# Kernel optimization log

Measured on AMD Instinct MI355X. Metric: run time of the kernel, lower is better.

Reference implementation:

```python
import jax, jax.numpy as jnp
import numpy as np

NA = 100000   # node_num_a
NB = 100000   # node_num_b
D = 128       # a_dim == b_dim
E = 1_600_000 # edges, avg degree 16


def setup_inputs() -> dict:
    key = jax.random.key(0)
    k1, k2, k3, k4, k5, k6 = jax.random.split(key, 6)
    feature_a = jax.random.normal(k1, (NA, D), dtype=jnp.float32)
    feature_b = jax.random.normal(k2, (NB, D), dtype=jnp.float32)
    src = jax.random.randint(k3, (E, 1), 0, NA)
    dst = jax.random.randint(k4, (E, 1), 0, NB)
    edges = jnp.concatenate([src, dst], axis=1).astype(jnp.int64)
    W_mlp = jax.random.normal(k5, (D, D), dtype=jnp.float32) / np.sqrt(D)
    b_mlp = jnp.zeros((D,), dtype=jnp.float32)
    a_vec = jax.random.normal(k6, (2 * D, 1), dtype=jnp.float32) / np.sqrt(2 * D)
    return {"feature_a": feature_a, "feature_b": feature_b, "edges": edges,
            "W_mlp": W_mlp, "b_mlp": b_mlp, "a_vec": a_vec}


def reference(feature_a, feature_b, edges, W_mlp, b_mlp, a_vec):
    """AttentionAggregator.forward: edge-gathered attention + segment aggregation."""
    na, a_dim = feature_a.shape
    # nn.Linear: x @ W.T + b
    new_emb = feature_b @ W_mlp.T + b_mlp                      # [Nb, D]
    # einsum(cat([fa[src], new_emb[dst]]), a) == fa[src]@a_top + new_emb[dst]@a_bot
    a_top = a_vec[:a_dim, 0]
    a_bot = a_vec[a_dim:, 0]
    s_a = feature_a @ a_top                                    # [Na]
    s_b = new_emb @ a_bot                                      # [Nb]
    src = edges[:, 0]
    dst = edges[:, 1]
    score = s_a[src] + s_b[dst]                                # [E]
    # F.elu(x, alpha=0.1) then exp
    ALPHA = 0.1
    elu = jnp.where(score > 0, score, ALPHA * jnp.expm1(score))
    w = jnp.exp(elu)                                           # [E]
    # sparse.mm(matrix, ones)  -> per-row sum of edge weights (duplicates coalesce by sum)
    row_sum = jax.ops.segment_sum(w, src, num_segments=na)     # [Na]
    row_sum = jnp.where(row_sum == 0, 1.0, row_sum)
    # sparse.mm(matrix, new_emb) -> weighted neighbor aggregation
    msg = w[:, None] * new_emb[dst]                            # [E, D]
    agg = jax.ops.segment_sum(msg, src, num_segments=na)       # [Na, D]
    return agg / row_sum[:, None]
```

## Files before the change

### kernel.cpp

```cpp
#include <hip/hip_runtime.h>
#include <math.h>

#define NA 100000
#define NB 100000
#define DIM 128
#define NEDGE 1600000
#define ALPHA 0.1f

#define WS_NEBF   0
#define WS_WBF    25600000
#define WS_SA     25632768
#define WS_SB     26032768
#define WS_DEG    26432768
#define WS_FLAG   26832768
#define WS_OFF    26832832
#define WS_CUR    27232832
#define WS_PAIRS  27632832

using bf16x8 = __attribute__((ext_vector_type(8))) short;
using f32x16 = __attribute__((ext_vector_type(16))) float;

__device__ inline short f2bf(float f) {
    union { float f; unsigned u; } v; v.f = f;
    const unsigned r = (v.u + 0x7FFFu + ((v.u >> 16) & 1u)) >> 16;
    return (short)r;
}

__global__ void k_prep(const int* __restrict__ edges32, int* __restrict__ flags,
                       const float* __restrict__ W, short* __restrict__ wbf) {
    if (blockIdx.x == 0) {
        __shared__ int any;
        if (threadIdx.x == 0) any = 0;
        __syncthreads();
        if (edges32[2 * threadIdx.x + 1] != 0) atomicOr(&any, 1);
        __syncthreads();
        if (threadIdx.x == 0) flags[0] = (any == 0) ? 1 : 0;
    } else {
        const int i = (blockIdx.x - 1) * 256 + threadIdx.x;
        if (i < DIM * DIM) wbf[i] = f2bf(W[i]);
    }
}

__global__ __launch_bounds__(256) void k_newemb(
    const float* __restrict__ fb, const short* __restrict__ wbf,
    const float* __restrict__ bias, const float* __restrict__ avec,
    short* __restrict__ nebf, float* __restrict__ s_b)
{
    const int wv = threadIdx.x >> 6;
    const int lane = threadIdx.x & 63;
    const int tile = blockIdx.x * 4 + wv;
    const int row0 = tile * 32;
    if (row0 >= NB) return;
    const int l31 = lane & 31;
    const int h = lane >> 5;

    f32x16 acc[4];
    #pragma unroll
    for (int nt = 0; nt < 4; ++nt)
        #pragma unroll
        for (int r = 0; r < 16; ++r) acc[nt][r] = 0.f;

    const float* arow = fb + (size_t)(row0 + l31) * DIM;

    #pragma unroll 2
    for (int s = 0; s < 8; ++s) {
        const int k0 = s * 16 + h * 8;
        const float4 a0 = *(const float4*)(arow + k0);
        const float4 a1 = *(const float4*)(arow + k0 + 4);
        bf16x8 af;
        af[0] = f2bf(a0.x); af[1] = f2bf(a0.y); af[2] = f2bf(a0.z); af[3] = f2bf(a0.w);
        af[4] = f2bf(a1.x); af[5] = f2bf(a1.y); af[6] = f2bf(a1.z); af[7] = f2bf(a1.w);
        #pragma unroll
        for (int nt = 0; nt < 4; ++nt) {
            const int n = nt * 32 + l31;
            const bf16x8 bf = *(const bf16x8*)(wbf + n * DIM + k0);
            acc[nt] = __builtin_amdgcn_mfma_f32_32x32x16_bf16(af, bf, acc[nt], 0, 0, 0);
        }
    }

    float ab[4], bs[4];
    #pragma unroll
    for (int nt = 0; nt < 4; ++nt) {
        ab[nt] = avec[DIM + nt * 32 + l31];
        bs[nt] = bias[nt * 32 + l31];
    }
    float sb[16];
    #pragma unroll
    for (int r = 0; r < 16; ++r) {
        const int row = row0 + (r & 3) + 8 * (r >> 2) + 4 * h;
        float p = 0.f;
        #pragma unroll
        for (int nt = 0; nt < 4; ++nt) {
            const float v = acc[nt][r] + bs[nt];
            nebf[(size_t)row * DIM + nt * 32 + l31] = f2bf(v);
            p += v * ab[nt];
        }
        #pragma unroll
        for (int m = 16; m; m >>= 1) p += __shfl_xor(p, m, 64);
        sb[r] = p;
    }
    if (l31 == 0) {
        #pragma unroll
        for (int r = 0; r < 16; ++r)
            s_b[row0 + (r & 3) + 8 * (r >> 2) + 4 * h] = sb[r];
    }
}

__global__ __launch_bounds__(256) void k_sa(
    const float* __restrict__ fa, const float* __restrict__ avec,
    float* __restrict__ s_a)
{
    const int row = blockIdx.x * 4 + (threadIdx.x >> 6);
    if (row >= NA) return;
    const int lane = threadIdx.x & 63;
    const float2 v = *(const float2*)(fa + (size_t)row * DIM + 2 * lane);
    const float2 a = *(const float2*)(avec + 2 * lane);
    float p = v.x * a.x + v.y * a.y;
    #pragma unroll
    for (int m = 32; m; m >>= 1) p += __shfl_xor(p, m, 64);
    if (lane == 0) s_a[row] = p;
}

__global__ __launch_bounds__(256) void k_hist(
    const void* __restrict__ edges, const int* __restrict__ flags,
    int* __restrict__ deg)
{
    const int e = blockIdx.x * 256 + threadIdx.x;
    if (e >= NEDGE) return;
    int src;
    if (flags[0]) src = (int)((const long long*)edges)[2 * (size_t)e];
    else          src = ((const int2*)edges)[e].x;
    atomicAdd(&deg[src], 1);
}

__global__ __launch_bounds__(256) void k_off(
    const int* __restrict__ deg, int* __restrict__ offs, int* __restrict__ cur,
    int* __restrict__ flags)
{
    const int lane = threadIdx.x & 63;
    const int w = blockIdx.x * 4 + (threadIdx.x >> 6);
    const int r = w * 64 + lane;
    const int d = (r < NA) ? deg[r] : 0;
    int incl = d;
    #pragma unroll
    for (int m = 1; m < 64; m <<= 1) {
        const int t = __shfl_up(incl, m, 64);
        if (lane >= m) incl += t;
    }
    int base = 0;
    if (lane == 63) base = atomicAdd(&flags[1], incl);
    base = __shfl(base, 63, 64);
    if (r < NA) {
        const int o = base + incl - d;
        offs[r] = o;
        cur[r] = o;
    }
}

__global__ __launch_bounds__(256) void k_place(
    const void* __restrict__ edges, const int* __restrict__ flags,
    const float* __restrict__ s_a, const float* __restrict__ s_b,
    int* __restrict__ cur, int2* __restrict__ pairs)
{
    const int e = blockIdx.x * 256 + threadIdx.x;
    if (e >= NEDGE) return;
    int src, dst;
    if (flags[0]) {
        const long long* p = (const long long*)edges;
        src = (int)p[2 * (size_t)e];
        dst = (int)p[2 * (size_t)e + 1];
    } else {
        const int2 ed = ((const int2*)edges)[e];
        src = ed.x; dst = ed.y;
    }
    const float sc = s_a[src] + s_b[dst];
    const float el = (sc > 0.f) ? sc : ALPHA * expm1f(sc);
    const float w = expf(el);
    const int pos = atomicAdd(&cur[src], 1);
    if ((unsigned)pos < NEDGE)
        pairs[pos] = make_int2(dst, __float_as_int(w));
}

#define ACC8(u, wt)                                                             \
    a0 += (wt) * __uint_as_float((u).x << 16);                                  \
    a1 += (wt) * __uint_as_float((u).x & 0xFFFF0000u);                          \
    a2 += (wt) * __uint_as_float((u).y << 16);                                  \
    a3 += (wt) * __uint_as_float((u).y & 0xFFFF0000u);                          \
    a4 += (wt) * __uint_as_float((u).z << 16);                                  \
    a5 += (wt) * __uint_as_float((u).z & 0xFFFF0000u);                          \
    a6 += (wt) * __uint_as_float((u).w << 16);                                  \
    a7 += (wt) * __uint_as_float((u).w & 0xFFFF0000u);

__global__ __launch_bounds__(256) void k_rowagg(
    const int* __restrict__ deg, const int* __restrict__ offs,
    const int2* __restrict__ pairs, const unsigned* __restrict__ nebf,
    float* __restrict__ out)
{
    const int row = blockIdx.x * 4 + (threadIdx.x >> 6);
    if (row >= NA) return;
    const int lane = threadIdx.x & 63;
    const int l = lane & 15;
    const int q = lane >> 4;
    const int cnt = deg[row];
    const int2* bucket = pairs + offs[row];

    float a0 = 0.f, a1 = 0.f, a2 = 0.f, a3 = 0.f;
    float a4 = 0.f, a5 = 0.f, a6 = 0.f, a7 = 0.f, wsum = 0.f;
    int i = q;
    for (; i + 4 < cnt; i += 8) {
        const int2 p0 = bucket[i];
        const int2 p1 = bucket[i + 4];
        const uint4 u0 = *(const uint4*)(nebf + (size_t)p0.x * (DIM / 2) + 4 * l);
        const uint4 u1 = *(const uint4*)(nebf + (size_t)p1.x * (DIM / 2) + 4 * l);
        const float w0 = __int_as_float(p0.y);
        const float w1 = __int_as_float(p1.y);
        ACC8(u0, w0)
        ACC8(u1, w1)
        wsum += w0 + w1;
    }
    for (; i < cnt; i += 4) {
        const int2 p = bucket[i];
        const uint4 u = *(const uint4*)(nebf + (size_t)p.x * (DIM / 2) + 4 * l);
        const float wv = __int_as_float(p.y);
        ACC8(u, wv)
        wsum += wv;
    }
    a0 += __shfl_xor(a0, 16, 64); a0 += __shfl_xor(a0, 32, 64);
    a1 += __shfl_xor(a1, 16, 64); a1 += __shfl_xor(a1, 32, 64);
    a2 += __shfl_xor(a2, 16, 64); a2 += __shfl_xor(a2, 32, 64);
    a3 += __shfl_xor(a3, 16, 64); a3 += __shfl_xor(a3, 32, 64);
    a4 += __shfl_xor(a4, 16, 64); a4 += __shfl_xor(a4, 32, 64);
    a5 += __shfl_xor(a5, 16, 64); a5 += __shfl_xor(a5, 32, 64);
    a6 += __shfl_xor(a6, 16, 64); a6 += __shfl_xor(a6, 32, 64);
    a7 += __shfl_xor(a7, 16, 64); a7 += __shfl_xor(a7, 32, 64);
    wsum += __shfl_xor(wsum, 16, 64); wsum += __shfl_xor(wsum, 32, 64);
    if (q == 0) {
        const float inv = 1.f / ((wsum == 0.f) ? 1.f : wsum);
        float* o = out + (size_t)row * DIM + 8 * l;
        *(float4*)o       = make_float4(a0 * inv, a1 * inv, a2 * inv, a3 * inv);
        *(float4*)(o + 4) = make_float4(a4 * inv, a5 * inv, a6 * inv, a7 * inv);
    }
}

extern "C" void kernel_launch(void* const* d_in, const int* in_sizes, int n_in,
                              void* d_out, int out_size, void* d_ws, size_t ws_size,
                              hipStream_t stream) {
    const float* fa    = (const float*)d_in[0];
    const float* fb    = (const float*)d_in[1];
    const void*  edges = d_in[2];
    const float* W     = (const float*)d_in[3];
    const float* bias  = (const float*)d_in[4];
    const float* avec  = (const float*)d_in[5];
    float* out = (float*)d_out;
    char* ws = (char*)d_ws;
    short* nebf = (short*)(ws + WS_NEBF);
    short* wbf  = (short*)(ws + WS_WBF);
    float* s_a  = (float*)(ws + WS_SA);
    float* s_b  = (float*)(ws + WS_SB);
    int*   deg  = (int*)(ws + WS_DEG);
    int*   flags= (int*)(ws + WS_FLAG);
    int*   offs = (int*)(ws + WS_OFF);
    int*   cur  = (int*)(ws + WS_CUR);
    int2*  pairs= (int2*)(ws + WS_PAIRS);

    (void)hipMemsetAsync(ws + WS_DEG, 0, (size_t)NA * sizeof(int) + 64, stream);
    k_prep<<<1 + (DIM * DIM + 255) / 256, 256, 0, stream>>>((const int*)edges, flags, W, wbf);
    k_newemb<<<(NB / 32 + 3) / 4, 256, 0, stream>>>(fb, wbf, bias, avec, nebf, s_b);
    k_sa<<<(NA + 3) / 4, 256, 0, stream>>>(fa, avec, s_a);
    k_hist<<<(NEDGE + 255) / 256, 256, 0, stream>>>(edges, flags, deg);
    k_off<<<(NA + 255) / 256, 256, 0, stream>>>(deg, offs, cur, flags);
    k_place<<<(NEDGE + 255) / 256, 256, 0, stream>>>(edges, flags, s_a, s_b, cur, pairs);
    k_rowagg<<<(NA + 3) / 4, 256, 0, stream>>>(deg, offs, pairs, (const unsigned*)nebf, out);
}
```

Baseline: 410.6 us.

## Fuse newemb, s_a and histogram kernels; drop cursor array; batch edges per thread

Result: slower. 446.6 us (+8.8%).

```diff
diff --git a/kernel.cpp b/kernel.cpp
--- a/kernel.cpp
+++ b/kernel.cpp
@@ -14,8 +14,14 @@
 #define WS_DEG    26432768
 #define WS_FLAG   26832768
 #define WS_OFF    26832832
-#define WS_CUR    27232832
-#define WS_PAIRS  27632832
+#define WS_PAIRS  27232832
+
+#define NEWEMB_BLOCKS 782
+#define SA_BLOCKS     25000
+#define EPT_H 8
+#define HIST_BLOCKS   782
+#define EPT_P 4
+#define PLACE_BLOCKS  1563
 
 using bf16x8 = __attribute__((ext_vector_type(8))) short;
 using f32x16 = __attribute__((ext_vector_type(16))) float;
@@ -41,101 +47,106 @@
     }
 }
 
-__global__ __launch_bounds__(256) void k_newemb(
+__global__ __launch_bounds__(256) void k_fused(
     const float* __restrict__ fb, const short* __restrict__ wbf,
     const float* __restrict__ bias, const float* __restrict__ avec,
-    short* __restrict__ nebf, float* __restrict__ s_b)
-{
-    const int wv = threadIdx.x >> 6;
-    const int lane = threadIdx.x & 63;
-    const int tile = blockIdx.x * 4 + wv;
-    const int row0 = tile * 32;
-    if (row0 >= NB) return;
-    const int l31 = lane & 31;
-    const int h = lane >> 5;
-
-    f32x16 acc[4];
-    #pragma unroll
-    for (int nt = 0; nt < 4; ++nt)
-        #pragma unroll
-        for (int r = 0; r < 16; ++r) acc[nt][r] = 0.f;
-
-    const float* arow = fb + (size_t)(row0 + l31) * DIM;
-
-    #pragma unroll 2
-    for (int s = 0; s < 8; ++s) {
-        const int k0 = s * 16 + h * 8;
-        const float4 a0 = *(const float4*)(arow + k0);
-        const float4 a1 = *(const float4*)(arow + k0 + 4);
-        bf16x8 af;
-        af[0] = f2bf(a0.x); af[1] = f2bf(a0.y); af[2] = f2bf(a0.z); af[3] = f2bf(a0.w);
-        af[4] = f2bf(a1.x); af[5] = f2bf(a1.y); af[6] = f2bf(a1.z); af[7] = f2bf(a1.w);
-        #pragma unroll
-        for (int nt = 0; nt < 4; ++nt) {
-            const int n = nt * 32 + l31;
-            const bf16x8 bf = *(const bf16x8*)(wbf + n * DIM + k0);
-            acc[nt] = __builtin_amdgcn_mfma_f32_32x32x16_bf16(af, bf, acc[nt], 0, 0, 0);
-        }
-    }
-
-    float ab[4], bs[4];
-    #pragma unroll
-    for (int nt = 0; nt < 4; ++nt) {
-        ab[nt] = avec[DIM + nt * 32 + l31];
-        bs[nt] = bias[nt * 32 + l31];
-    }
-    float sb[16];
-    #pragma unroll
-    for (int r = 0; r < 16; ++r) {
-        const int row = row0 + (r & 3) + 8 * (r >> 2) + 4 * h;
-        float p = 0.f;
-        #pragma unroll
-        for (int nt = 0; nt < 4; ++nt) {
-            const float v = acc[nt][r] + bs[nt];
-            nebf[(size_t)row * DIM + nt * 32 + l31] = f2bf(v);
-            p += v * ab[nt];
-        }
-        #pragma unroll
-        for (int m = 16; m; m >>= 1) p += __shfl_xor(p, m, 64);
-        sb[r] = p;
-    }
-    if (l31 == 0) {
-        #pragma unroll
-        for (int r = 0; r < 16; ++r)
-            s_b[row0 + (r & 3) + 8 * (r >> 2) + 4 * h] = sb[r];
-    }
-}
-
-__global__ __launch_bounds__(256) void k_sa(
-    const float* __restrict__ fa, const float* __restrict__ avec,
-    float* __restrict__ s_a)
-{
-    const int row = blockIdx.x * 4 + (threadIdx.x >> 6);
-    if (row >= NA) return;
-    const int lane = threadIdx.x & 63;
-    const float2 v = *(const float2*)(fa + (size_t)row * DIM + 2 * lane);
-    const float2 a = *(const float2*)(avec + 2 * lane);
-    float p = v.x * a.x + v.y * a.y;
-    #pragma unroll
-    for (int m = 32; m; m >>= 1) p += __shfl_xor(p, m, 64);
-    if (lane == 0) s_a[row] = p;
-}
-
-__global__ __launch_bounds__(256) void k_hist(
+    short* __restrict__ nebf, float* __restrict__ s_b,
+    const float* __restrict__ fa, float* __restrict__ s_a,
     const void* __restrict__ edges, const int* __restrict__ flags,
     int* __restrict__ deg)
 {
-    const int e = blockIdx.x * 256 + threadIdx.x;
-    if (e >= NEDGE) return;
-    int src;
-    if (flags[0]) src = (int)((const long long*)edges)[2 * (size_t)e];
-    else          src = ((const int2*)edges)[e].x;
-    atomicAdd(&deg[src], 1);
+    const int lane = threadIdx.x & 63;
+    if (blockIdx.x < NEWEMB_BLOCKS) {
+        const int wv = threadIdx.x >> 6;
+        const int tile = blockIdx.x * 4 + wv;
+        const int row0 = tile * 32;
+        if (row0 >= NB) return;
+        const int l31 = lane & 31;
+        const int h = lane >> 5;
+
+        f32x16 acc[4];
+        #pragma unroll
+        for (int nt = 0; nt < 4; ++nt)
+            #pragma unroll
+            for (int r = 0; r < 16; ++r) acc[nt][r] = 0.f;
+
+        const float* arow = fb + (size_t)(row0 + l31) * DIM;
+
+        #pragma unroll 2
+        for (int s = 0; s < 8; ++s) {
+            const int k0 = s * 16 + h * 8;
+            const float4 a0 = *(const float4*)(arow + k0);
+            const float4 a1 = *(const float4*)(arow + k0 + 4);
+            bf16x8 af;
+            af[0] = f2bf(a0.x); af[1] = f2bf(a0.y); af[2] = f2bf(a0.z); af[3] = f2bf(a0.w);
+            af[4] = f2bf(a1.x); af[5] = f2bf(a1.y); af[6] = f2bf(a1.z); af[7] = f2bf(a1.w);
+            #pragma unroll
+            for (int nt = 0; nt < 4; ++nt) {
+                const int n = nt * 32 + l31;
+                const bf16x8 bf = *(const bf16x8*)(wbf + n * DIM + k0);
+                acc[nt] = __builtin_amdgcn_mfma_f32_32x32x16_bf16(af, bf, acc[nt], 0, 0, 0);
+            }
+        }
+
+        float ab[4], bs[4];
+        #pragma unroll
+        for (int nt = 0; nt < 4; ++nt) {
+            ab[nt] = avec[DIM + nt * 32 + l31];
+            bs[nt] = bias[nt * 32 + l31];
+        }
+        float sb[16];
+        #pragma unroll
+        for (int r = 0; r < 16; ++r) {
+            const int row = row0 + (r & 3) + 8 * (r >> 2) + 4 * h;
+            float p = 0.f;
+            #pragma unroll
+            for (int nt = 0; nt < 4; ++nt) {
+                const float v = acc[nt][r] + bs[nt];
+                nebf[(size_t)row * DIM + nt * 32 + l31] = f2bf(v);
+                p += v * ab[nt];
+            }
+            #pragma unroll
+            for (int m = 16; m; m >>= 1) p += __shfl_xor(p, m, 64);
+            sb[r] = p;
+        }
+        if (l31 == 0) {
+            #pragma unroll
+            for (int r = 0; r < 16; ++r)
+                s_b[row0 + (r & 3) + 8 * (r >> 2) + 4 * h] = sb[r];
+        }
+    } else if (blockIdx.x < NEWEMB_BLOCKS + SA_BLOCKS) {
+        const int row = (blockIdx.x - NEWEMB_BLOCKS) * 4 + (threadIdx.x >> 6);
+        if (row >= NA) return;
+        const float2 v = *(const float2*)(fa + (size_t)row * DIM + 2 * lane);
+        const float2 a = *(const float2*)(avec + 2 * lane);
+        float p = v.x * a.x + v.y * a.y;
+        #pragma unroll
+        for (int m = 32; m; m >>= 1) p += __shfl_xor(p, m, 64);
+        if (lane == 0) s_a[row] = p;
+    } else {
+        const int t = (blockIdx.x - NEWEMB_BLOCKS - SA_BLOCKS) * 256 + threadIdx.x;
+        const long long e0 = (long long)t * EPT_H;
+        if (e0 >= NEDGE) return;
+        if (flags[0]) {
+            const int4* p = (const int4*)edges;
+            int s[EPT_H];
+            #pragma unroll
+            for (int k = 0; k < EPT_H; ++k) s[k] = p[e0 + k].x;
+            #pragma unroll
+            for (int k = 0; k < EPT_H; ++k) atomicAdd(&deg[s[k]], 1);
+        } else {
+            const int2* p = (const int2*)edges;
+            int s[EPT_H];
+            #pragma unroll
+            for (int k = 0; k < EPT_H; ++k) s[k] = p[e0 + k].x;
+            #pragma unroll
+            for (int k = 0; k < EPT_H; ++k) atomicAdd(&deg[s[k]], 1);
+        }
+    }
 }
 
 __global__ __launch_bounds__(256) void k_off(
-    const int* __restrict__ deg, int* __restrict__ offs, int* __restrict__ cur,
-    int* __restrict__ flags)
+    const int* __restrict__ deg, int* __restrict__ offs, int* __restrict__ flags)
 {
     const int lane = threadIdx.x & 63;
     const int w = blockIdx.x * 4 + (threadIdx.x >> 6);
@@ -150,35 +161,41 @@
     int base = 0;
     if (lane == 63) base = atomicAdd(&flags[1], incl);
     base = __shfl(base, 63, 64);
-    if (r < NA) {
-        const int o = base + incl - d;
-        offs[r] = o;
-        cur[r] = o;
-    }
+    if (r < NA) offs[r] = base + incl - d;
 }
 
 __global__ __launch_bounds__(256) void k_place(
     const void* __restrict__ edges, const int* __restrict__ flags,
     const float* __restrict__ s_a, const float* __restrict__ s_b,
-    int* __restrict__ cur, int2* __restrict__ pairs)
-{
-    const int e = blockIdx.x * 256 + threadIdx.x;
-    if (e >= NEDGE) return;
-    int src, dst;
+    int* __restrict__ offs, int2* __restrict__ pairs)
+{
+    const int t = blockIdx.x * 256 + threadIdx.x;
+    const long long e0 = (long long)t * EPT_P;
+    if (e0 >= NEDGE) return;
+    int src[EPT_P], dst[EPT_P];
     if (flags[0]) {
-        const long long* p = (const long long*)edges;
-        src = (int)p[2 * (size_t)e];
-        dst = (int)p[2 * (size_t)e + 1];
+        const int4* p = (const int4*)edges;
+        #pragma unroll
+        for (int k = 0; k < EPT_P; ++k) { const int4 v = p[e0 + k]; src[k] = v.x; dst[k] = v.z; }
     } else {
-        const int2 ed = ((const int2*)edges)[e];
-        src = ed.x; dst = ed.y;
-    }
-    const float sc = s_a[src] + s_b[dst];
-    const float el = (sc > 0.f) ? sc : ALPHA * expm1f(sc);
-    const float w = expf(el);
-    const int pos = atomicAdd(&cur[src], 1);
-    if ((unsigned)pos < NEDGE)
-        pairs[pos] = make_int2(dst, __float_as_int(w));
+        const int2* p = (const int2*)edges;
+        #pragma unroll
+        for (int k = 0; k < EPT_P; ++k) { const int2 v = p[e0 + k]; src[k] = v.x; dst[k] = v.y; }
+    }
+    float w[EPT_P];
+    #pragma unroll
+    for (int k = 0; k < EPT_P; ++k) {
+        const float sc = s_a[src[k]] + s_b[dst[k]];
+        const float el = (sc > 0.f) ? sc : ALPHA * expm1f(sc);
+        w[k] = expf(el);
+    }
+    int pos[EPT_P];
+    #pragma unroll
+    for (int k = 0; k < EPT_P; ++k) pos[k] = atomicAdd(&offs[src[k]], 1);
+    #pragma unroll
+    for (int k = 0; k < EPT_P; ++k)
+        if ((unsigned)pos[k] < NEDGE)
+            pairs[pos[k]] = make_int2(dst[k], __float_as_int(w[k]));
 }
 
 #define ACC8(u, wt)                                                             \
@@ -202,7 +219,7 @@
     const int l = lane & 15;
     const int q = lane >> 4;
     const int cnt = deg[row];
-    const int2* bucket = pairs + offs[row];
+    const int2* bucket = pairs + (offs[row] - cnt);
 
     float a0 = 0.f, a1 = 0.f, a2 = 0.f, a3 = 0.f;
     float a4 = 0.f, a5 = 0.f, a6 = 0.f, a7 = 0.f, wsum = 0.f;
@@ -260,15 +277,13 @@
     int*   deg  = (int*)(ws + WS_DEG);
     int*   flags= (int*)(ws + WS_FLAG);
     int*   offs = (int*)(ws + WS_OFF);
-    int*   cur  = (int*)(ws + WS_CUR);
     int2*  pairs= (int2*)(ws + WS_PAIRS);
 
     (void)hipMemsetAsync(ws + WS_DEG, 0, (size_t)NA * sizeof(int) + 64, stream);
     k_prep<<<1 + (DIM * DIM + 255) / 256, 256, 0, stream>>>((const int*)edges, flags, W, wbf);
-    k_newemb<<<(NB / 32 + 3) / 4, 256, 0, stream>>>(fb, wbf, bias, avec, nebf, s_b);
-    k_sa<<<(NA + 3) / 4, 256, 0, stream>>>(fa, avec, s_a);
-    k_hist<<<(NEDGE + 255) / 256, 256, 0, stream>>>(edges, flags, deg);
-    k_off<<<(NA + 255) / 256, 256, 0, stream>>>(deg, offs, cur, flags);
-    k_place<<<(NEDGE + 255) / 256, 256, 0, stream>>>(edges, flags, s_a, s_b, cur, pairs);
+    k_fused<<<NEWEMB_BLOCKS + SA_BLOCKS + HIST_BLOCKS, 256, 0, stream>>>(
+        fb, wbf, bias, avec, nebf, s_b, fa, s_a, edges, flags, deg);
+    k_off<<<(NA + 255) / 256, 256, 0, stream>>>(deg, offs, flags);
+    k_place<<<PLACE_BLOCKS, 256, 0, stream>>>(edges, flags, s_a, s_b, offs, pairs);
     k_rowagg<<<(NA + 3) / 4, 256, 0, stream>>>(deg, offs, pairs, (const unsigned*)nebf, out);
 }
```

## Replace CSR build with fixed-capacity per-row buckets and overflow list

Applied to the files above, without the earlier changes.

Result: slower. 424.8 us (+3.4%).

```diff
diff --git a/kernel.cpp b/kernel.cpp
--- a/kernel.cpp
+++ b/kernel.cpp
@@ -6,16 +6,20 @@
 #define DIM 128
 #define NEDGE 1600000
 #define ALPHA 0.1f
+#define BCAP 31
+#define OVF_CAP 65536
 
 #define WS_NEBF   0
 #define WS_WBF    25600000
 #define WS_SA     25632768
 #define WS_SB     26032768
-#define WS_DEG    26432768
+#define WS_CNT    26432768
 #define WS_FLAG   26832768
-#define WS_OFF    26832832
-#define WS_CUR    27232832
-#define WS_PAIRS  27632832
+#define WS_OVF    26832832
+#define WS_PAIRS  27357120
+
+#define EPT_P 4
+#define SCAT_BLOCKS 1563
 
 using bf16x8 = __attribute__((ext_vector_type(8))) short;
 using f32x16 = __attribute__((ext_vector_type(16))) float;
@@ -121,64 +125,36 @@
     if (lane == 0) s_a[row] = p;
 }
 
-__global__ __launch_bounds__(256) void k_hist(
+__global__ __launch_bounds__(256) void k_scatter(
     const void* __restrict__ edges, const int* __restrict__ flags,
-    int* __restrict__ deg)
-{
-    const int e = blockIdx.x * 256 + threadIdx.x;
-    if (e >= NEDGE) return;
-    int src;
-    if (flags[0]) src = (int)((const long long*)edges)[2 * (size_t)e];
-    else          src = ((const int2*)edges)[e].x;
-    atomicAdd(&deg[src], 1);
-}
-
-__global__ __launch_bounds__(256) void k_off(
-    const int* __restrict__ deg, int* __restrict__ offs, int* __restrict__ cur,
-    int* __restrict__ flags)
-{
-    const int lane = threadIdx.x & 63;
-    const int w = blockIdx.x * 4 + (threadIdx.x >> 6);
-    const int r = w * 64 + lane;
-    const int d = (r < NA) ? deg[r] : 0;
-    int incl = d;
-    #pragma unroll
-    for (int m = 1; m < 64; m <<= 1) {
-        const int t = __shfl_up(incl, m, 64);
-        if (lane >= m) incl += t;
-    }
-    int base = 0;
-    if (lane == 63) base = atomicAdd(&flags[1], incl);
-    base = __shfl(base, 63, 64);
-    if (r < NA) {
-        const int o = base + incl - d;
-        offs[r] = o;
-        cur[r] = o;
-    }
-}
-
-__global__ __launch_bounds__(256) void k_place(
-    const void* __restrict__ edges, const int* __restrict__ flags,
-    const float* __restrict__ s_a, const float* __restrict__ s_b,
-    int* __restrict__ cur, int2* __restrict__ pairs)
-{
-    const int e = blockIdx.x * 256 + threadIdx.x;
-    if (e >= NEDGE) return;
-    int src, dst;
+    int* __restrict__ cnt, int* __restrict__ bucket,
+    int2* __restrict__ ovf, int* __restrict__ ovfcnt)
+{
+    const int t = blockIdx.x * 256 + threadIdx.x;
+    const long long e0 = (long long)t * EPT_P;
+    if (e0 >= NEDGE) return;
+    int src[EPT_P], dst[EPT_P];
     if (flags[0]) {
-        const long long* p = (const long long*)edges;
-        src = (int)p[2 * (size_t)e];
-        dst = (int)p[2 * (size_t)e + 1];
+        const int4* p = (const int4*)edges;
+        #pragma unroll
+        for (int k = 0; k < EPT_P; ++k) { const int4 v = p[e0 + k]; src[k] = v.x; dst[k] = v.z; }
     } else {
-        const int2 ed = ((const int2*)edges)[e];
-        src = ed.x; dst = ed.y;
-    }
-    const float sc = s_a[src] + s_b[dst];
-    const float el = (sc > 0.f) ? sc : ALPHA * expm1f(sc);
-    const float w = expf(el);
-    const int pos = atomicAdd(&cur[src], 1);
-    if ((unsigned)pos < NEDGE)
-        pairs[pos] = make_int2(dst, __float_as_int(w));
+        const int2* p = (const int2*)edges;
+        #pragma unroll
+        for (int k = 0; k < EPT_P; ++k) { const int2 v = p[e0 + k]; src[k] = v.x; dst[k] = v.y; }
+    }
+    int pos[EPT_P];
+    #pragma unroll
+    for (int k = 0; k < EPT_P; ++k) pos[k] = atomicAdd(&cnt[src[k]], 1);
+    #pragma unroll
+    for (int k = 0; k < EPT_P; ++k) {
+        if (pos[k] < BCAP) {
+            bucket[src[k] * BCAP + pos[k]] = dst[k];
+        } else {
+            const int o = atomicAdd(ovfcnt, 1);
+            if (o < OVF_CAP) ovf[o] = make_int2(src[k], dst[k]);
+        }
+    }
 }
 
 #define ACC8(u, wt)                                                             \
@@ -191,39 +167,59 @@
     a6 += (wt) * __uint_as_float((u).w << 16);                                  \
     a7 += (wt) * __uint_as_float((u).w & 0xFFFF0000u);
 
+__device__ inline float edge_w(float sar, float sb) {
+    const float sc = sar + sb;
+    const float el = (sc > 0.f) ? sc : ALPHA * expm1f(sc);
+    return expf(el);
+}
+
 __global__ __launch_bounds__(256) void k_rowagg(
-    const int* __restrict__ deg, const int* __restrict__ offs,
-    const int2* __restrict__ pairs, const unsigned* __restrict__ nebf,
-    float* __restrict__ out)
+    const int* __restrict__ cnt, const int* __restrict__ bucket_all,
+    const float* __restrict__ s_a, const float* __restrict__ s_b,
+    const unsigned* __restrict__ nebf, const int2* __restrict__ ovf,
+    const int* __restrict__ flags, float* __restrict__ out)
 {
     const int row = blockIdx.x * 4 + (threadIdx.x >> 6);
     if (row >= NA) return;
     const int lane = threadIdx.x & 63;
     const int l = lane & 15;
     const int q = lane >> 4;
-    const int cnt = deg[row];
-    const int2* bucket = pairs + offs[row];
+    const int c = cnt[row];
+    const int cb = (c > BCAP) ? BCAP : c;
+    const int* bucket = bucket_all + row * BCAP;
+    const float sar = s_a[row];
 
     float a0 = 0.f, a1 = 0.f, a2 = 0.f, a3 = 0.f;
     float a4 = 0.f, a5 = 0.f, a6 = 0.f, a7 = 0.f, wsum = 0.f;
     int i = q;
-    for (; i + 4 < cnt; i += 8) {
-        const int2 p0 = bucket[i];
-        const int2 p1 = bucket[i + 4];
-        const uint4 u0 = *(const uint4*)(nebf + (size_t)p0.x * (DIM / 2) + 4 * l);
-        const uint4 u1 = *(const uint4*)(nebf + (size_t)p1.x * (DIM / 2) + 4 * l);
-        const float w0 = __int_as_float(p0.y);
-        const float w1 = __int_as_float(p1.y);
+    for (; i + 4 < cb; i += 8) {
+        const int d0 = bucket[i];
+        const int d1 = bucket[i + 4];
+        const uint4 u0 = *(const uint4*)(nebf + (size_t)d0 * (DIM / 2) + 4 * l);
+        const uint4 u1 = *(const uint4*)(nebf + (size_t)d1 * (DIM / 2) + 4 * l);
+        const float w0 = edge_w(sar, s_b[d0]);
+        const float w1 = edge_w(sar, s_b[d1]);
         ACC8(u0, w0)
         ACC8(u1, w1)
         wsum += w0 + w1;
     }
-    for (; i < cnt; i += 4) {
-        const int2 p = bucket[i];
-        const uint4 u = *(const uint4*)(nebf + (size_t)p.x * (DIM / 2) + 4 * l);
-        const float wv = __int_as_float(p.y);
+    for (; i < cb; i += 4) {
+        const int d = bucket[i];
+        const uint4 u = *(const uint4*)(nebf + (size_t)d * (DIM / 2) + 4 * l);
+        const float wv = edge_w(sar, s_b[d]);
         ACC8(u, wv)
         wsum += wv;
+    }
+    int novf = flags[1];
+    novf = (novf > OVF_CAP) ? OVF_CAP : novf;
+    for (int j = q; j < novf; j += 4) {
+        const int2 pe = ovf[j];
+        if (pe.x == row) {
+            const uint4 u = *(const uint4*)(nebf + (size_t)pe.y * (DIM / 2) + 4 * l);
+            const float wv = edge_w(sar, s_b[pe.y]);
+            ACC8(u, wv)
+            wsum += wv;
+        }
     }
     a0 += __shfl_xor(a0, 16, 64); a0 += __shfl_xor(a0, 32, 64);
     a1 += __shfl_xor(a1, 16, 64); a1 += __shfl_xor(a1, 32, 64);
@@ -253,22 +249,20 @@
     const float* avec  = (const float*)d_in[5];
     float* out = (float*)d_out;
     char* ws = (char*)d_ws;
-    short* nebf = (short*)(ws + WS_NEBF);
-    short* wbf  = (short*)(ws + WS_WBF);
-    float* s_a  = (float*)(ws + WS_SA);
-    float* s_b  = (float*)(ws + WS_SB);
-    int*   deg  = (int*)(ws + WS_DEG);
-    int*   flags= (int*)(ws + WS_FLAG);
-    int*   offs = (int*)(ws + WS_OFF);
-    int*   cur  = (int*)(ws + WS_CUR);
-    int2*  pairs= (int2*)(ws + WS_PAIRS);
-
-    (void)hipMemsetAsync(ws + WS_DEG, 0, (size_t)NA * sizeof(int) + 64, stream);
+    short* nebf  = (short*)(ws + WS_NEBF);
+    short* wbf   = (short*)(ws + WS_WBF);
+    float* s_a   = (float*)(ws + WS_SA);
+    float* s_b   = (float*)(ws + WS_SB);
+    int*   cnt   = (int*)(ws + WS_CNT);
+    int*   flags = (int*)(ws + WS_FLAG);
+    int2*  ovf   = (int2*)(ws + WS_OVF);
+    int*   bucket= (int*)(ws + WS_PAIRS);
+
+    (void)hipMemsetAsync(ws + WS_CNT, 0, (size_t)NA * sizeof(int) + 64, stream);
     k_prep<<<1 + (DIM * DIM + 255) / 256, 256, 0, stream>>>((const int*)edges, flags, W, wbf);
     k_newemb<<<(NB / 32 + 3) / 4, 256, 0, stream>>>(fb, wbf, bias, avec, nebf, s_b);
     k_sa<<<(NA + 3) / 4, 256, 0, stream>>>(fa, avec, s_a);
-    k_hist<<<(NEDGE + 255) / 256, 256, 0, stream>>>(edges, flags, deg);
-    k_off<<<(NA + 255) / 256, 256, 0, stream>>>(deg, offs, cur, flags);
-    k_place<<<(NEDGE + 255) / 256, 256, 0, stream>>>(edges, flags, s_a, s_b, cur, pairs);
-    k_rowagg<<<(NA + 3) / 4, 256, 0, stream>>>(deg, offs, pairs, (const unsigned*)nebf, out);
-}
+    k_scatter<<<SCAT_BLOCKS, 256, 0, stream>>>(edges, flags, cnt, bucket, ovf, &flags[1]);
+    k_rowagg<<<(NA + 3) / 4, 256, 0, stream>>>(cnt, bucket, s_a, s_b,
+                                               (const unsigned*)nebf, ovf, flags, out);
+}
```
